# Kernel optimization log

Hardware: AMD Instinct MI355X
Metric: run time of the kernel (lower is better)

## Reference

```python
import jax, jax.numpy as jnp
import numpy as np

B, LX, LY, D = 8, 2048, 2048, 256

def setup_inputs() -> dict:
    key = jax.random.key(0)
    k1, k2, k3, k4 = jax.random.split(key, 4)
    x = jax.random.normal(k1, (B, LX, D), dtype=jnp.float32)
    y = jax.random.normal(k2, (B, LY, D), dtype=jnp.float32)
    y_mask = jax.random.randint(k3, (B, LY), 0, 2).astype(jnp.bool_)
    W = jax.random.normal(k4, (D, D), dtype=jnp.float32) * (1.0 / np.sqrt(D))
    b = jnp.zeros((D,), dtype=jnp.float32)
    return {"x": x, "y": y, "y_mask": y_mask, "W": W, "b": b}

def reference(x, y, y_mask, W, b):
    # shared linear + relu projection (torch Linear: x @ W.T + b)
    x_proj = jax.nn.relu(jnp.einsum('bld,ed->ble', x, W) + b)  # [B,LX,D]
    y_proj = jax.nn.relu(jnp.einsum('bld,ed->ble', y, W) + b)  # [B,LY,D]
    scores = jnp.einsum('bxd,byd->bxy', x_proj, y_proj)        # [B,LX,LY]
    scores = jnp.where(y_mask[:, None, :], -jnp.inf, scores)
    alpha = jax.nn.softmax(scores, axis=-1)                    # [B,LX,LY]
    return jnp.einsum('bxy,byd->bxd', alpha, y)                # [B,LX,D]
```

## Files before the change

kernel.cpp:

```cpp
#include <hip/hip_runtime.h>

typedef __attribute__((ext_vector_type(8))) short short8;
typedef _Float16 half8 __attribute__((ext_vector_type(8)));
typedef __attribute__((ext_vector_type(4))) float f32x4;
typedef __attribute__((ext_vector_type(4))) unsigned int uint4v;
typedef __attribute__((ext_vector_type(2))) unsigned int uint2v;

#define B_   8
#define LX_  2048
#define LY_  2048
#define D_   256
#define NROW (B_ * LX_)

__device__ __forceinline__ unsigned short f2bf(float f) {
  unsigned u = __builtin_bit_cast(unsigned, f);
  u += 0x7FFF + ((u >> 16) & 1);
  return (unsigned short)(u >> 16);
}
__device__ __forceinline__ float bf2f(unsigned short h) {
  unsigned u = ((unsigned)h) << 16;
  return __builtin_bit_cast(float, u);
}

__global__ __launch_bounds__(256) void prep_kernel(
    const float* __restrict__ W, unsigned short* __restrict__ Whi,
    unsigned short* __restrict__ Wlo,
    const int* __restrict__ MASK, int* __restrict__ CIDX, int* __restrict__ Lc) {
  int t = threadIdx.x;
  if (blockIdx.x >= 8) {
    int base = (blockIdx.x - 8) * 2048 + t * 8;
    f32x4 f0 = *(const f32x4*)(W + base);
    f32x4 f1 = *(const f32x4*)(W + base + 4);
    float v[8] = {f0[0], f0[1], f0[2], f0[3], f1[0], f1[1], f1[2], f1[3]};
    unsigned short h[8], l[8];
    for (int j = 0; j < 8; ++j) {
      h[j] = f2bf(v[j]);
      l[j] = f2bf(v[j] - bf2f(h[j]));
    }
    uint4v vh = {(unsigned)h[0] | ((unsigned)h[1] << 16), (unsigned)h[2] | ((unsigned)h[3] << 16),
                 (unsigned)h[4] | ((unsigned)h[5] << 16), (unsigned)h[6] | ((unsigned)h[7] << 16)};
    uint4v vl = {(unsigned)l[0] | ((unsigned)l[1] << 16), (unsigned)l[2] | ((unsigned)l[3] << 16),
                 (unsigned)l[4] | ((unsigned)l[5] << 16), (unsigned)l[6] | ((unsigned)l[7] << 16)};
    *(uint4v*)(Whi + base) = vh;
    *(uint4v*)(Wlo + base) = vl;
    return;
  }
  __shared__ int s[256];
  int b = blockIdx.x;
  int f[8];
  int cnt = 0;
  for (int k = 0; k < 8; ++k) {
    f[k] = (MASK[b * 2048 + t * 8 + k] == 0) ? 1 : 0;
    cnt += f[k];
  }
  s[t] = cnt;
  __syncthreads();
  for (int off = 1; off < 256; off <<= 1) {
    int v = (t >= off) ? s[t - off] : 0;
    __syncthreads();
    s[t] += v;
    __syncthreads();
  }
  if (t == 255) Lc[b] = s[255];
  int off = s[t] - cnt;
  for (int k = 0; k < 8; ++k) {
    int j = t * 8 + k;
    if (f[k]) CIDX[b * 2048 + (off++)] = j;
  }
}

__global__ __launch_bounds__(256, 2) void projgather_kernel(
    const float* __restrict__ X, const float* __restrict__ Y,
    const float* __restrict__ bias,
    const unsigned short* __restrict__ Whi, const unsigned short* __restrict__ Wlo,
    const int* __restrict__ CIDX, const int* __restrict__ Lc,
    _Float16* __restrict__ XP, _Float16* __restrict__ YPc,
    _Float16* __restrict__ YTc) {
  __shared__ __align__(16) unsigned char smem[51200];
  int t = threadIdx.x;

  if (blockIdx.x >= 512) {
    _Float16 (*tile)[72] = (_Float16(*)[72])smem;
    int id = blockIdx.x - 512;
    int db = id & 3, nb = (id >> 2) & 31, b = id >> 7;
    int lc = Lc[b];
    int end = (lc + 31) & ~31;
    if (nb * 64 >= end) return;
    int nl = t >> 2, ds = t & 3;
    int j = nb * 64 + nl;
    int idx = (j < lc) ? CIDX[b * 2048 + j] : 0;
    const float* src = Y + (size_t)(b * LY_ + idx) * D_ + db * 64 + ds * 16;
    for (int i = 0; i < 4; ++i) {
      f32x4 f = *(const f32x4*)(src + i * 4);
      for (int k = 0; k < 4; ++k) tile[ds * 16 + i * 4 + k][nl] = (_Float16)f[k];
    }
    __syncthreads();
    int dl = t >> 2, nsub = t & 3;
    uint4v v0 = *(const uint4v*)&tile[dl][nsub * 16];
    uint4v v1 = *(const uint4v*)&tile[dl][nsub * 16 + 8];
    _Float16* dst = YTc + (size_t)(b * D_ + db * 64 + dl) * LY_ + nb * 64 + nsub * 16;
    *(uint4v*)(dst) = v0;
    *(uint4v*)(dst + 8) = v1;
    return;
  }

  unsigned short (*Ah)[40] = (unsigned short(*)[40])(smem);
  unsigned short (*Al)[40] = (unsigned short(*)[40])(smem + 5120);
  unsigned short (*Bh)[40] = (unsigned short(*)[40])(smem + 10240);
  unsigned short (*Bl)[40] = (unsigned short(*)[40])(smem + 30720);

  int lane = t & 63, wave = t >> 6;
  int q = lane >> 4, n15 = lane & 15;
  int arow = t >> 2, aseg = t & 3;
  int erow = t >> 2, ec = t & 3;

  bool isX = blockIdx.x < 256;
  int m0 = 0, b = 0, slot0 = 0, lcb = 0;
  const float* arow_ptr;
  if (isX) {
    m0 = blockIdx.x * 64;
    arow_ptr = X + (size_t)(m0 + arow) * D_;
  } else {
    int id = blockIdx.x - 256;
    b = id >> 5;
    int rb = id & 31;
    lcb = Lc[b];
    slot0 = rb * 64;
    if (slot0 >= lcb) return;
    int sl = slot0 + arow;
    int grow = (sl < lcb) ? CIDX[b * 2048 + sl] : 0;
    arow_ptr = Y + (size_t)(b * 2048 + grow) * D_;
  }

  f32x4 acc[4][4];
  for (int mt = 0; mt < 4; ++mt)
    for (int nt = 0; nt < 4; ++nt) acc[mt][nt] = (f32x4){0.f, 0.f, 0.f, 0.f};

  f32x4 pa[2];
  uint4v pbh[4], pbl[4];
#define PROJ_PF(kc)                                                            \
  {                                                                            \
    for (int i = 0; i < 2; ++i)                                                \
      pa[i] = *(const f32x4*)(arow_ptr + (kc) * 32 + (aseg + i * 4) * 4);      \
    for (int p = 0; p < 4; ++p) {                                              \
      int e = p * 64 + erow;                                                   \
      pbh[p] = *(const uint4v*)(Whi + (size_t)e * D_ + (kc) * 32 + ec * 8);    \
      pbl[p] = *(const uint4v*)(Wlo + (size_t)e * D_ + (kc) * 32 + ec * 8);    \
    }                                                                          \
  }

  PROJ_PF(0);

  for (int kc = 0; kc < 8; ++kc) {
    __syncthreads();
    for (int i = 0; i < 2; ++i) {
      int seg = aseg + i * 4;
      f32x4 f = pa[i];
      unsigned short h[4], l[4];
      for (int j = 0; j < 4; ++j) {
        h[j] = f2bf(f[j]);
        l[j] = f2bf(f[j] - bf2f(h[j]));
      }
      uint2v vh = {(unsigned)h[0] | ((unsigned)h[1] << 16),
                   (unsigned)h[2] | ((unsigned)h[3] << 16)};
      uint2v vl = {(unsigned)l[0] | ((unsigned)l[1] << 16),
                   (unsigned)l[2] | ((unsigned)l[3] << 16)};
      *(uint2v*)&Ah[arow][seg * 4] = vh;
      *(uint2v*)&Al[arow][seg * 4] = vl;
    }
    for (int p = 0; p < 4; ++p) {
      int e = p * 64 + erow;
      *(uint4v*)&Bh[e][ec * 8] = pbh[p];
      *(uint4v*)&Bl[e][ec * 8] = pbl[p];
    }
    if (kc < 7) PROJ_PF(kc + 1);
    __syncthreads();

    short8 afh[4], afl[4], bfh[4], bfl[4];
    for (int mt = 0; mt < 4; ++mt) {
      afh[mt] = *(const short8*)&Ah[mt * 16 + n15][q * 8];
      afl[mt] = *(const short8*)&Al[mt * 16 + n15][q * 8];
    }
    for (int nt = 0; nt < 4; ++nt) {
      bfh[nt] = *(const short8*)&Bh[wave * 64 + nt * 16 + n15][q * 8];
      bfl[nt] = *(const short8*)&Bl[wave * 64 + nt * 16 + n15][q * 8];
    }
    for (int mt = 0; mt < 4; ++mt)
      for (int nt = 0; nt < 4; ++nt) {
        acc[mt][nt] = __builtin_amdgcn_mfma_f32_16x16x32_bf16(afh[mt], bfh[nt], acc[mt][nt], 0, 0, 0);
        acc[mt][nt] = __builtin_amdgcn_mfma_f32_16x16x32_bf16(afl[mt], bfh[nt], acc[mt][nt], 0, 0, 0);
        acc[mt][nt] = __builtin_amdgcn_mfma_f32_16x16x32_bf16(afh[mt], bfl[nt], acc[mt][nt], 0, 0, 0);
      }
  }
#undef PROJ_PF

  __syncthreads();
  _Float16 (*epi)[264] = (_Float16(*)[264])smem;
  for (int nt = 0; nt < 4; ++nt) {
    int e = wave * 64 + nt * 16 + n15;
    float bv = bias[e];
    for (int mt = 0; mt < 4; ++mt)
      for (int r = 0; r < 4; ++r) {
        float v = acc[mt][nt][r] + bv;
        v = v > 0.f ? v : 0.f;
        epi[mt * 16 + q * 4 + r][e] = (_Float16)v;
      }
  }
  __syncthreads();
  int row = t >> 2, seg = t & 3;
  bool valid = isX || (slot0 + row < lcb);
  if (valid) {
    _Float16* drp = isX ? (XP + (size_t)(m0 + row) * D_)
                        : (YPc + (size_t)(b * 2048 + slot0 + row) * D_);
    for (int k = 0; k < 8; ++k) {
      uint4v v = *(const uint4v*)&epi[row][seg * 64 + k * 8];
      *(uint4v*)(drp + seg * 64 + k * 8) = v;
    }
  }
}

__global__ __launch_bounds__(256, 2) void flash_kernel(
    const _Float16* __restrict__ XP, const _Float16* __restrict__ YPc,
    const _Float16* __restrict__ YTc, const int* __restrict__ Lc,
    _Float16* __restrict__ PO, float* __restrict__ Pm, float* __restrict__ Pl) {
  __shared__ __align__(16) _Float16 yp_t[64][264];
  __shared__ __align__(16) _Float16 yT_t[256][64];
  __shared__ __align__(16) _Float16 pbuf[4][16][72];

  int t = threadIdx.x;
  int lane = t & 63, wave = t >> 6;
  int q = lane >> 4, n15 = lane & 15;
  int half = blockIdx.x & 1;
  int xb = (blockIdx.x >> 1) & 31;
  int b = blockIdx.x >> 6;
  int row0 = xb * 64 + wave * 16;

  int lc = Lc[b];
  int T  = (lc + 63) >> 6;
  int tstart = (T * half) >> 1;
  int tend   = (T * (half + 1)) >> 1;

  half8 a[8];
  const _Float16* xrow = XP + (size_t)(b * LX_ + row0 + n15) * D_ + q * 8;
  for (int kk = 0; kk < 8; ++kk) a[kk] = *(const half8*)(xrow + kk * 32);

  float m_r[4];
  for (int r = 0; r < 4; ++r) m_r[r] = -1e30f;
  f32x4 lacc = {0.f, 0.f, 0.f, 0.f};
  f32x4 oacc[16];
  for (int dt = 0; dt < 16; ++dt) oacc[dt] = (f32x4){0.f, 0.f, 0.f, 0.f};

  const _Float16* ypb = YPc + (size_t)b * LY_ * D_;
  const _Float16* yTb = YTc + (size_t)b * D_ * LY_;

  uint4v pr[16];
#define PREFETCH(tt)                                                          \
  {                                                                           \
    int y0p = (tt) * 64;                                                      \
    for (int i = 0; i < 8; ++i) {                                             \
      int c = t + i * 256;                                                    \
      pr[i] = *(const uint4v*)(ypb + (size_t)(y0p + (c >> 5)) * D_ + (c & 31) * 8); \
    }                                                                         \
    for (int i = 0; i < 8; ++i) {                                             \
      int c = t + i * 256;                                                    \
      pr[8 + i] = *(const uint4v*)(yTb + (size_t)(c >> 3) * LY_ + y0p + (c & 7) * 8); \
    }                                                                         \
  }

  if (tstart < tend) PREFETCH(tstart);

  for (int tt = tstart; tt < tend; ++tt) {
    int y0 = tt * 64;
    __syncthreads();
    for (int i = 0; i < 8; ++i) {
      int c = t + i * 256;
      *(uint4v*)&yp_t[c >> 5][(c & 31) * 8] = pr[i];
    }
    for (int i = 0; i < 8; ++i) {
      int c = t + i * 256;
      int rT = c >> 3, pc = (c & 7) ^ (rT & 7);
      *(uint4v*)&yT_t[rT][pc * 8] = pr[8 + i];
    }
    if (tt + 1 < tend) PREFETCH(tt + 1);
    __syncthreads();

    f32x4 S0 = {0.f, 0.f, 0.f, 0.f}, S1 = {0.f, 0.f, 0.f, 0.f};
    f32x4 S2 = {0.f, 0.f, 0.f, 0.f}, S3 = {0.f, 0.f, 0.f, 0.f};
    for (int kk = 0; kk < 8; ++kk) {
      half8 b0 = *(const half8*)&yp_t[n15][kk * 32 + q * 8];
      half8 b1 = *(const half8*)&yp_t[16 + n15][kk * 32 + q * 8];
      half8 b2 = *(const half8*)&yp_t[32 + n15][kk * 32 + q * 8];
      half8 b3 = *(const half8*)&yp_t[48 + n15][kk * 32 + q * 8];
      S0 = __builtin_amdgcn_mfma_f32_16x16x32_f16(a[kk], b0, S0, 0, 0, 0);
      S1 = __builtin_amdgcn_mfma_f32_16x16x32_f16(a[kk], b1, S1, 0, 0, 0);
      S2 = __builtin_amdgcn_mfma_f32_16x16x32_f16(a[kk], b2, S2, 0, 0, 0);
      S3 = __builtin_amdgcn_mfma_f32_16x16x32_f16(a[kk], b3, S3, 0, 0, 0);
    }
    bool mk0 = (y0 + n15) >= lc;
    bool mk1 = (y0 + 16 + n15) >= lc;
    bool mk2 = (y0 + 32 + n15) >= lc;
    bool mk3 = (y0 + 48 + n15) >= lc;

    f32x4 alv;
    bool need = false;
#pragma unroll
    for (int r = 0; r < 4; ++r) {
      float s0 = mk0 ? -1e30f : S0[r];
      float s1 = mk1 ? -1e30f : S1[r];
      float s2 = mk2 ? -1e30f : S2[r];
      float s3 = mk3 ? -1e30f : S3[r];
      float tm = fmaxf(fmaxf(s0, s1), fmaxf(s2, s3));
      tm = fmaxf(tm, __shfl_xor(tm, 1));
      tm = fmaxf(tm, __shfl_xor(tm, 2));
      tm = fmaxf(tm, __shfl_xor(tm, 4));
      tm = fmaxf(tm, __shfl_xor(tm, 8));
      float mn = fmaxf(m_r[r], tm);
      float al = __expf(m_r[r] - mn);
      m_r[r] = mn;
      float p0 = __expf(s0 - mn);
      float p1 = __expf(s1 - mn);
      float p2 = __expf(s2 - mn);
      float p3 = __expf(s3 - mn);
      pbuf[wave][q * 4 + r][n15]      = (_Float16)p0;
      pbuf[wave][q * 4 + r][16 + n15] = (_Float16)p1;
      pbuf[wave][q * 4 + r][32 + n15] = (_Float16)p2;
      pbuf[wave][q * 4 + r][48 + n15] = (_Float16)p3;
      lacc[r] = lacc[r] * al + (p0 + p1) + (p2 + p3);
      alv[r] = al;
      need = need || (al != 1.0f);
    }
    if (__ballot(need)) {
      for (int dt = 0; dt < 16; ++dt)
        for (int r = 0; r < 4; ++r) oacc[dt][r] *= alv[r];
    }
    half8 pa0 = *(const half8*)&pbuf[wave][n15][q * 8];
    half8 pa1 = *(const half8*)&pbuf[wave][n15][32 + q * 8];
    for (int dt = 0; dt < 16; ++dt) {
      int rT = dt * 16 + n15, x = rT & 7;
      half8 bb0 = *(const half8*)&yT_t[rT][(q ^ x) * 8];
      half8 bb1 = *(const half8*)&yT_t[rT][((4 + q) ^ x) * 8];
      oacc[dt] = __builtin_amdgcn_mfma_f32_16x16x32_f16(pa0, bb0, oacc[dt], 0, 0, 0);
      oacc[dt] = __builtin_amdgcn_mfma_f32_16x16x32_f16(pa1, bb1, oacc[dt], 0, 0, 0);
    }
  }
#undef PREFETCH

  size_t prow = (size_t)(half * B_ + b) * LX_ + row0;
  _Float16* po = PO + prow * D_;
  for (int dt = 0; dt < 16; ++dt)
    for (int r = 0; r < 4; ++r)
      po[(size_t)(q * 4 + r) * D_ + dt * 16 + n15] = (_Float16)oacc[dt][r];
  for (int r = 0; r < 4; ++r) {
    float v = lacc[r];
    v += __shfl_xor(v, 1);
    v += __shfl_xor(v, 2);
    v += __shfl_xor(v, 4);
    v += __shfl_xor(v, 8);
    lacc[r] = v;
  }
  if (n15 == 0) {
    for (int r = 0; r < 4; ++r) {
      Pm[prow + q * 4 + r] = m_r[r];
      Pl[prow + q * 4 + r] = lacc[r];
    }
  }
}

__global__ __launch_bounds__(256) void merge_kernel(
    const _Float16* __restrict__ PO, const float* __restrict__ Pm,
    const float* __restrict__ Pl, float* __restrict__ OUT) {
  int c = blockIdx.x * 256 + threadIdx.x;
  int row = c >> 5, seg = c & 31;
  float m0 = Pm[row], m1 = Pm[NROW + row];
  float l0 = Pl[row], l1 = Pl[NROW + row];
  float m = fmaxf(m0, m1);
  float w0 = __expf(m0 - m), w1 = __expf(m1 - m);
  float inv = 1.0f / (l0 * w0 + l1 * w1);
  const _Float16* p0 = PO + (size_t)row * D_ + seg * 8;
  const _Float16* p1 = p0 + (size_t)NROW * D_;
  half8 a = *(const half8*)p0;
  half8 bsec = *(const half8*)p1;
  float* o = OUT + (size_t)row * D_ + seg * 8;
  f32x4 o0, o1;
  for (int j = 0; j < 4; ++j) o0[j] = ((float)a[j] * w0 + (float)bsec[j] * w1) * inv;
  for (int j = 0; j < 4; ++j) o1[j] = ((float)a[4 + j] * w0 + (float)bsec[4 + j] * w1) * inv;
  *(f32x4*)o = o0;
  *(f32x4*)(o + 4) = o1;
}

extern "C" void kernel_launch(void* const* d_in, const int* in_sizes, int n_in,
                              void* d_out, int out_size, void* d_ws, size_t ws_size,
                              hipStream_t stream) {
  const float* x     = (const float*)d_in[0];
  const float* y     = (const float*)d_in[1];
  const int*   ymask = (const int*)  d_in[2];
  const float* W     = (const float*)d_in[3];
  const float* bias  = (const float*)d_in[4];
  float* out = (float*)d_out;

  char* ws = (char*)d_ws;
  size_t o = 0;
  unsigned short* Whi = (unsigned short*)(ws + o); o += 131072;
  unsigned short* Wlo = (unsigned short*)(ws + o); o += 131072;
  _Float16* XP  = (_Float16*)(ws + o); o += 8388608;
  _Float16* YPc = (_Float16*)(ws + o); o += 8388608;
  _Float16* YTc = (_Float16*)(ws + o); o += 8388608;
  _Float16* PO  = (_Float16*)(ws + o); o += 16777216;
  float* Pm   = (float*)(ws + o); o += 131072;
  float* Pl   = (float*)(ws + o); o += 131072;
  int*   CIDX = (int*)  (ws + o); o += 65536;
  int*   Lc   = (int*)  (ws + o);

  prep_kernel<<<40, 256, 0, stream>>>(W, Whi, Wlo, ymask, CIDX, Lc);
  projgather_kernel<<<1536, 256, 0, stream>>>(x, y, bias, Whi, Wlo, CIDX, Lc,
                                              XP, YPc, YTc);
  flash_kernel<<<512, 256, 0, stream>>>(XP, YPc, YTc, Lc, PO, Pm, Pl);
  merge_kernel<<<2048, 256, 0, stream>>>(PO, Pm, Pl, out);
}
```

Before: 152.6 us.

## Fuse split-softmax merge into flash kernel via last-block atomic counter

Measured after the change: 228.3 us. +49.6%, slower.

```diff
diff --git a/kernel.cpp b/kernel.cpp
--- a/kernel.cpp
+++ b/kernel.cpp
@@ -25,9 +25,11 @@
 __global__ __launch_bounds__(256) void prep_kernel(
     const float* __restrict__ W, unsigned short* __restrict__ Whi,
     unsigned short* __restrict__ Wlo,
-    const int* __restrict__ MASK, int* __restrict__ CIDX, int* __restrict__ Lc) {
+    const int* __restrict__ MASK, int* __restrict__ CIDX, int* __restrict__ Lc,
+    unsigned* __restrict__ FLAG) {
   int t = threadIdx.x;
   if (blockIdx.x >= 8) {
+    if (blockIdx.x == 8) FLAG[t] = 0u;
     int base = (blockIdx.x - 8) * 2048 + t * 8;
     f32x4 f0 = *(const f32x4*)(W + base);
     f32x4 f1 = *(const f32x4*)(W + base + 4);
@@ -222,7 +224,8 @@
 __global__ __launch_bounds__(256, 2) void flash_kernel(
     const _Float16* __restrict__ XP, const _Float16* __restrict__ YPc,
     const _Float16* __restrict__ YTc, const int* __restrict__ Lc,
-    _Float16* __restrict__ PO, float* __restrict__ Pm, float* __restrict__ Pl) {
+    _Float16* __restrict__ PO, float* __restrict__ Pm, float* __restrict__ Pl,
+    unsigned* __restrict__ FLAG, float* __restrict__ OUT) {
   __shared__ __align__(16) _Float16 yp_t[64][264];
   __shared__ __align__(16) _Float16 yT_t[256][64];
   __shared__ __align__(16) _Float16 pbuf[4][16][72];
@@ -364,28 +367,38 @@
       Pl[prow + q * 4 + r] = lacc[r];
     }
   }
-}
-
-__global__ __launch_bounds__(256) void merge_kernel(
-    const _Float16* __restrict__ PO, const float* __restrict__ Pm,
-    const float* __restrict__ Pl, float* __restrict__ OUT) {
-  int c = blockIdx.x * 256 + threadIdx.x;
-  int row = c >> 5, seg = c & 31;
-  float m0 = Pm[row], m1 = Pm[NROW + row];
-  float l0 = Pl[row], l1 = Pl[NROW + row];
-  float m = fmaxf(m0, m1);
-  float w0 = __expf(m0 - m), w1 = __expf(m1 - m);
-  float inv = 1.0f / (l0 * w0 + l1 * w1);
-  const _Float16* p0 = PO + (size_t)row * D_ + seg * 8;
-  const _Float16* p1 = p0 + (size_t)NROW * D_;
-  half8 a = *(const half8*)p0;
-  half8 bsec = *(const half8*)p1;
-  float* o = OUT + (size_t)row * D_ + seg * 8;
-  f32x4 o0, o1;
-  for (int j = 0; j < 4; ++j) o0[j] = ((float)a[j] * w0 + (float)bsec[j] * w1) * inv;
-  for (int j = 0; j < 4; ++j) o1[j] = ((float)a[4 + j] * w0 + (float)bsec[4 + j] * w1) * inv;
-  *(f32x4*)o = o0;
-  *(f32x4*)(o + 4) = o1;
+
+  __syncthreads();
+  __shared__ unsigned lastv;
+  if (t == 0) {
+    __threadfence();
+    lastv = atomicAdd(&FLAG[b * 32 + xb], 1u);
+  }
+  __syncthreads();
+  if (lastv == 1u) {
+    __threadfence();
+    int rowbase = b * LX_ + xb * 64;
+    for (int i = 0; i < 8; ++i) {
+      int c = t + i * 256;
+      int row = rowbase + (c >> 5);
+      int seg = c & 31;
+      float m0 = Pm[row], m1 = Pm[NROW + row];
+      float l0 = Pl[row], l1 = Pl[NROW + row];
+      float m = fmaxf(m0, m1);
+      float w0 = __expf(m0 - m), w1 = __expf(m1 - m);
+      float inv = 1.0f / (l0 * w0 + l1 * w1);
+      const _Float16* p0 = PO + (size_t)row * D_ + seg * 8;
+      const _Float16* p1 = p0 + (size_t)NROW * D_;
+      half8 av = *(const half8*)p0;
+      half8 bv = *(const half8*)p1;
+      float* o = OUT + (size_t)row * D_ + seg * 8;
+      f32x4 o0, o1;
+      for (int j = 0; j < 4; ++j) o0[j] = ((float)av[j] * w0 + (float)bv[j] * w1) * inv;
+      for (int j = 0; j < 4; ++j) o1[j] = ((float)av[4 + j] * w0 + (float)bv[4 + j] * w1) * inv;
+      *(f32x4*)o = o0;
+      *(f32x4*)(o + 4) = o1;
+    }
+  }
 }
 
 extern "C" void kernel_launch(void* const* d_in, const int* in_sizes, int n_in,
@@ -409,11 +422,11 @@
   float* Pm   = (float*)(ws + o); o += 131072;
   float* Pl   = (float*)(ws + o); o += 131072;
   int*   CIDX = (int*)  (ws + o); o += 65536;
-  int*   Lc   = (int*)  (ws + o);
-
-  prep_kernel<<<40, 256, 0, stream>>>(W, Whi, Wlo, ymask, CIDX, Lc);
+  int*   Lc   = (int*)  (ws + o); o += 4096;
+  unsigned* FLAG = (unsigned*)(ws + o);
+
+  prep_kernel<<<40, 256, 0, stream>>>(W, Whi, Wlo, ymask, CIDX, Lc, FLAG);
   projgather_kernel<<<1536, 256, 0, stream>>>(x, y, bias, Whi, Wlo, CIDX, Lc,
                                               XP, YPc, YTc);
-  flash_kernel<<<512, 256, 0, stream>>>(XP, YPc, YTc, Lc, PO, Pm, Pl);
-  merge_kernel<<<2048, 256, 0, stream>>>(PO, Pm, Pl, out);
-}
+  flash_kernel<<<512, 256, 0, stream>>>(XP, YPc, YTc, Lc, PO, Pm, Pl, FLAG, out);
+}
```
